# Optimization experiments

Hardware: AMD Instinct MI355X
Metric: run time of the kernel (lower is better)

## Reference

```python
import jax, jax.numpy as jnp
import numpy as np

N_NODES = 100000


def _gcn_layer(x, src, dst, W, b, num_nodes):
    # Linear transform first (PyG GCNConv applies Linear before propagate).
    h = x @ W.T  # [N, out]
    # Degree (with self loops already included in src/dst), computed on target.
    ones = jnp.ones(dst.shape[0], dtype=h.dtype)
    deg = jax.ops.segment_sum(ones, dst, num_segments=num_nodes)
    dinv = jnp.where(deg > 0, jax.lax.rsqrt(deg), 0.0)
    norm = dinv[src] * dinv[dst]  # [E]
    msg = h[src] * norm[:, None]  # gather + per-edge scale, [E, out]
    out = jax.ops.segment_sum(msg, dst, num_segments=num_nodes)
    return out + b


def setup_inputs() -> dict:
    key = jax.random.key(0)
    k1, k2, k3, k4, k5, k6 = jax.random.split(key, 6)
    d = 64
    x = jax.random.normal(k1, (N_NODES, d), dtype=jnp.float32)
    edge_index = jax.random.randint(k2, (2, 1600000), 0, N_NODES, dtype=jnp.int64)
    s = 1.0 / np.sqrt(d)
    W1 = jax.random.normal(k3, (d, d), dtype=jnp.float32) * s
    b1 = jax.random.normal(k4, (d,), dtype=jnp.float32) * 0.01
    W2 = jax.random.normal(k5, (d, d), dtype=jnp.float32) * s
    b2 = jax.random.normal(k6, (d,), dtype=jnp.float32) * 0.01
    return {"x": x, "edge_index": edge_index, "W1": W1, "b1": b1, "W2": W2, "b2": b2}


def reference(x, edge_index, W1, b1, W2, b2):
    n = x.shape[0]
    loop = jnp.arange(n, dtype=edge_index.dtype)
    src = jnp.concatenate([edge_index[0], loop])  # add self loops
    dst = jnp.concatenate([edge_index[1], loop])
    h = _gcn_layer(x, src, dst, W1, b1, n)
    out = _gcn_layer(h, src, dst, W2, b2, n)
    return out
```

## Files before the change

kernel.cpp:

```cpp
#include <hip/hip_runtime.h>
#include <hip/hip_fp16.h>


#define D 64
#define NPB 128
#define MAXB 784
#define CHUNK 4096
#define BT 512
#define CAP 3072

__global__ __launch_bounds__(BT) void build_scatter(const int* __restrict__ src,
                                                    const int* __restrict__ dst,
                                                    int* __restrict__ bcur,
                                                    int* __restrict__ entries0,
                                                    int nE, int B) {
    __shared__ int hist[MAXB];
    __shared__ int curs[MAXB];
    const int t = threadIdx.x;
    const int c = blockIdx.x;
    for (int b = t; b < B; b += BT) hist[b] = 0;
    __syncthreads();
    int e0 = c * CHUNK;
    int sv[CHUNK / BT], dv[CHUNK / BT];
#pragma unroll
    for (int i = 0; i < CHUNK / BT; ++i) {
        int e = e0 + i * BT + t;
        sv[i] = 0; dv[i] = -1;
        if (e < nE) {
            sv[i] = src[e];
            dv[i] = dst[e];
            atomicAdd(&hist[dv[i] >> 7], 1);
        }
    }
    __syncthreads();
    for (int b = t; b < B; b += BT) {
        int cnt = hist[b];
        int base = 0;
        if (cnt > 0) base = atomicAdd(&bcur[b], cnt);
        curs[b] = b * CAP + base;
    }
    __syncthreads();
#pragma unroll
    for (int i = 0; i < CHUNK / BT; ++i) {
        if (dv[i] >= 0) {
            int b = dv[i] >> 7;
            int pos = atomicAdd(&curs[b], 1);
            entries0[pos] = sv[i] | ((dv[i] & (NPB - 1)) << 17);
        }
    }
}

__device__ __forceinline__ void regroup_body(const int* __restrict__ entries0,
                                             int s0, int s1,
                                             int* __restrict__ off,
                                             int* __restrict__ deg,
                                             float* __restrict__ dinv,
                                             int* __restrict__ entries1,
                                             int* __restrict__ cursor, int N, int b,
                                             int* cnt, int* scn, int* cur, int* shb) {
    int t = threadIdx.x;
    if (t < NPB) cnt[t] = 0;
    if (t == 0) *shb = atomicAdd(cursor, s1 - s0);
    __syncthreads();
    for (int p = s0 + t; p < s1; p += 256)
        atomicAdd(&cnt[(entries0[p] >> 17) & (NPB - 1)], 1);
    __syncthreads();
    if (t < NPB) scn[t] = cnt[t];
    __syncthreads();
    for (int s = 1; s < NPB; s <<= 1) {
        int u = 0;
        if (t < NPB && t >= s) u = scn[t - s];
        __syncthreads();
        if (t < NPB) scn[t] += u;
        __syncthreads();
    }
    if (t < NPB) {
        int node = b * NPB + t;
        int c = cnt[t];
        int o = *shb + scn[t] - c;
        cur[t] = o;
        if (node < N) {
            off[node]  = o;
            deg[node]  = c;
            dinv[node] = rsqrtf((float)c + 1.0f);
        }
    }
    __syncthreads();
    for (int p = s0 + t; p < s1; p += 256) {
        int e = entries0[p];
        int pos = atomicAdd(&cur[(e >> 17) & (NPB - 1)], 1);
        entries1[pos] = e & 0x1FFFF;
    }
}

template <typename InT>
__device__ __forceinline__ void gemm_body(const InT* __restrict__ X,
                                          const float* __restrict__ W,
                                          const float* __restrict__ scale,
                                          __half* __restrict__ H, int N, int bx,
                                          float* xt, float* wt) {
    const int t = threadIdx.x;
    const int i0 = bx * 64;
#pragma unroll
    for (int r = 0; r < 16; ++r) {
        int idx = r * 256 + t;
        int j = idx >> 6, k = idx & 63;
        wt[k * 68 + j] = W[idx];
    }
#pragma unroll
    for (int r = 0; r < 16; ++r) {
        int idx = r * 256 + t;
        int i = idx >> 6, k = idx & 63;
        float v = 0.0f;
        if (i0 + i < N) {
            if constexpr (sizeof(InT) == 2)
                v = __half2float(((const __half*)X)[(size_t)(i0 + i) * D + k]);
            else
                v = ((const float*)X)[(size_t)(i0 + i) * D + k];
        }
        xt[k * 68 + i] = v;
    }
    __syncthreads();
    const int tn = (t & 15) * 4;
    const int tc = (t >> 4) * 4;
    float acc[4][4] = {};
#pragma unroll 8
    for (int k = 0; k < 64; ++k) {
        const float4 xa = *(const float4*)(xt + k * 68 + tn);
        const float4 wb = *(const float4*)(wt + k * 68 + tc);
        acc[0][0] += xa.x * wb.x; acc[0][1] += xa.x * wb.y; acc[0][2] += xa.x * wb.z; acc[0][3] += xa.x * wb.w;
        acc[1][0] += xa.y * wb.x; acc[1][1] += xa.y * wb.y; acc[1][2] += xa.y * wb.z; acc[1][3] += xa.y * wb.w;
        acc[2][0] += xa.z * wb.x; acc[2][1] += xa.z * wb.y; acc[2][2] += xa.z * wb.z; acc[2][3] += xa.z * wb.w;
        acc[3][0] += xa.w * wb.x; acc[3][1] += xa.w * wb.y; acc[3][2] += xa.w * wb.z; acc[3][3] += xa.w * wb.w;
    }
#pragma unroll
    for (int a = 0; a < 4; ++a) {
        int i = i0 + tn + a;
        if (i < N) {
            float sc = scale ? scale[i] : 1.0f;
            union { __half2 h2[2]; uint2 u2; } pk;
            pk.h2[0].x = __float2half_rn(acc[a][0] * sc);
            pk.h2[0].y = __float2half_rn(acc[a][1] * sc);
            pk.h2[1].x = __float2half_rn(acc[a][2] * sc);
            pk.h2[1].y = __float2half_rn(acc[a][3] * sc);
            *(uint2*)(&H[(size_t)i * D + tc]) = pk.u2;
        }
    }
}

__global__ __launch_bounds__(256) void regroup_gemm1(const int* __restrict__ entries0,
                                                     const int* __restrict__ btot,
                                                     int* __restrict__ off,
                                                     int* __restrict__ deg,
                                                     float* __restrict__ dinv,
                                                     int* __restrict__ entries1,
                                                     int* __restrict__ cursor,
                                                     int N, int B,
                                                     const float* __restrict__ X,
                                                     const float* __restrict__ W1,
                                                     __half* __restrict__ Hh) {
    __shared__ float xt[64 * 68];
    __shared__ float wt[64 * 68];
    if ((int)blockIdx.x < B) {
        int b = blockIdx.x;
        int* cnt = (int*)xt;
        int* scn = cnt + NPB;
        int* cur = scn + NPB;
        int* shb = cur + NPB;
        regroup_body(entries0, b * CAP, b * CAP + btot[b], off, deg, dinv,
                     entries1, cursor, N, b, cnt, scn, cur, shb);
    } else {
        gemm_body<float>(X, W1, nullptr, Hh, N, (int)blockIdx.x - B, xt, wt);
    }
}

template <bool PRESCALED>
__device__ __forceinline__ float2 agg_node(const int* __restrict__ csr, int beg, int end,
                                           const __half2* __restrict__ H2,
                                           const float* __restrict__ dinv,
                                           float dd, int p2, int h) {
    float2 acc = make_float2(0.0f, 0.0f);
    int p = beg;
    for (; p + 16 <= end; p += 16) {
        int s[8];
#pragma unroll
        for (int i = 0; i < 8; ++i) s[i] = csr[p + 2 * i + h];
        __half2 g[8];
#pragma unroll
        for (int i = 0; i < 8; ++i) g[i] = H2[(size_t)s[i] * 32 + p2];
        if constexpr (PRESCALED) {
#pragma unroll
            for (int i = 0; i < 8; ++i) {
                float2 f = __half22float2(g[i]);
                acc.x += f.x; acc.y += f.y;
            }
        } else {
            float dv[8];
#pragma unroll
            for (int i = 0; i < 8; ++i) dv[i] = dinv[s[i]];
#pragma unroll
            for (int i = 0; i < 8; ++i) {
                float2 f = __half22float2(g[i]);
                float c = dv[i] * dd;
                acc.x += f.x * c; acc.y += f.y * c;
            }
        }
    }
    for (; p + 8 <= end; p += 8) {
        int s0v = csr[p + 0 + h], s1v = csr[p + 2 + h];
        int s2v = csr[p + 4 + h], s3v = csr[p + 6 + h];
        __half2 g0 = H2[(size_t)s0v * 32 + p2];
        __half2 g1 = H2[(size_t)s1v * 32 + p2];
        __half2 g2 = H2[(size_t)s2v * 32 + p2];
        __half2 g3 = H2[(size_t)s3v * 32 + p2];
        float2 f0 = __half22float2(g0), f1 = __half22float2(g1);
        float2 f2 = __half22float2(g2), f3 = __half22float2(g3);
        if constexpr (PRESCALED) {
            acc.x += f0.x + f1.x + f2.x + f3.x;
            acc.y += f0.y + f1.y + f2.y + f3.y;
        } else {
            float c0 = dinv[s0v] * dd, c1 = dinv[s1v] * dd;
            float c2 = dinv[s2v] * dd, c3 = dinv[s3v] * dd;
            acc.x += f0.x * c0; acc.y += f0.y * c0;
            acc.x += f1.x * c1; acc.y += f1.y * c1;
            acc.x += f2.x * c2; acc.y += f2.y * c2;
            acc.x += f3.x * c3; acc.y += f3.y * c3;
        }
    }
    for (; p + 2 <= end; p += 2) {
        int s0v = csr[p + h];
        __half2 g0 = H2[(size_t)s0v * 32 + p2];
        float2 f0 = __half22float2(g0);
        if constexpr (PRESCALED) {
            acc.x += f0.x; acc.y += f0.y;
        } else {
            float c0 = dinv[s0v] * dd;
            acc.x += f0.x * c0; acc.y += f0.y * c0;
        }
    }
    if (p < end && h == 0) {
        int s0v = csr[p];
        __half2 g0 = H2[(size_t)s0v * 32 + p2];
        float2 f0 = __half22float2(g0);
        if constexpr (PRESCALED) {
            acc.x += f0.x; acc.y += f0.y;
        } else {
            float c0 = dinv[s0v] * dd;
            acc.x += f0.x * c0; acc.y += f0.y * c0;
        }
    }
    return acc;
}

template <typename OutT, bool PRESCALED>
__global__ __launch_bounds__(256) void aggregate3(const int* __restrict__ csr,
                                                  const int* __restrict__ off,
                                                  const int* __restrict__ deg,
                                                  const float* __restrict__ dinv,
                                                  const __half* __restrict__ H,
                                                  const float* __restrict__ bias,
                                                  OutT* __restrict__ out, int N) {
    int node = blockIdx.x * 4 + (threadIdx.x >> 6);
    if (node >= N) return;
    int lane = threadIdx.x & 63;
    int p2 = lane & 31;
    int h  = lane >> 5;
    const __half2* H2 = (const __half2*)H;
    float dd = dinv[node];
    int beg = off[node];
    int end = beg + deg[node];
    float2 acc = agg_node<PRESCALED>(csr, beg, end, H2, dinv, dd, p2, h);
    acc.x += __shfl_xor(acc.x, 32);
    acc.y += __shfl_xor(acc.y, 32);
    if (h == 0) {
        float2 hs = __half22float2(H2[(size_t)node * 32 + p2]);
        float2 bv = ((const float2*)bias)[p2];
        float2 o;
        if constexpr (PRESCALED) {
            o.x = (acc.x + hs.x) * dd + bv.x;
            o.y = (acc.y + hs.y) * dd + bv.y;
        } else {
            float s = dd * dd;
            o.x = acc.x + bv.x + hs.x * s;
            o.y = acc.y + bv.y + hs.y * s;
        }
        if constexpr (sizeof(OutT) == 2) {
            ((__half2*)(out + (size_t)node * D))[p2] = __float22half2_rn(o);
        } else {
            ((float2*)(out + (size_t)node * D))[p2] = o;
        }
    }
}

__global__ __launch_bounds__(256) void agg1_gemm2(const int* __restrict__ csr,
                                                  const int* __restrict__ off,
                                                  const int* __restrict__ deg,
                                                  const float* __restrict__ dinv,
                                                  const __half* __restrict__ H1,
                                                  const float* __restrict__ b1,
                                                  const float* __restrict__ W2,
                                                  __half* __restrict__ H2out, int N) {
    __shared__ float xt[64 * 68];
    __shared__ float wt[64 * 68];
    const int t = threadIdx.x;
#pragma unroll
    for (int r = 0; r < 16; ++r) {
        int idx = r * 256 + t;
        int j = idx >> 6, k = idx & 63;
        wt[k * 68 + j] = W2[idx];
    }
    const int i0 = blockIdx.x * 64;
    const int w = t >> 6, lane = t & 63, p2 = lane & 31, h = lane >> 5;
    const __half2* H2 = (const __half2*)H1;
    float2 bv = ((const float2*)b1)[p2];
    for (int r = 0; r < 16; ++r) {
        int il = w * 16 + r;
        int node = i0 + il;
        if (node < N) {
            float dd = dinv[node];
            int beg = off[node];
            int end = beg + deg[node];
            float2 acc = agg_node<false>(csr, beg, end, H2, dinv, dd, p2, h);
            acc.x += __shfl_xor(acc.x, 32);
            acc.y += __shfl_xor(acc.y, 32);
            if (h == 0) {
                float s = dd * dd;
                float2 hs = __half22float2(H2[(size_t)node * 32 + p2]);
                xt[(2 * p2)     * 68 + il] = acc.x + bv.x + hs.x * s;
                xt[(2 * p2 + 1) * 68 + il] = acc.y + bv.y + hs.y * s;
            }
        }
    }
    __syncthreads();
    const int tn = (t & 15) * 4;
    const int tc = (t >> 4) * 4;
    float acc[4][4] = {};
#pragma unroll 8
    for (int k = 0; k < 64; ++k) {
        const float4 xa = *(const float4*)(xt + k * 68 + tn);
        const float4 wb = *(const float4*)(wt + k * 68 + tc);
        acc[0][0] += xa.x * wb.x; acc[0][1] += xa.x * wb.y; acc[0][2] += xa.x * wb.z; acc[0][3] += xa.x * wb.w;
        acc[1][0] += xa.y * wb.x; acc[1][1] += xa.y * wb.y; acc[1][2] += xa.y * wb.z; acc[1][3] += xa.y * wb.w;
        acc[2][0] += xa.z * wb.x; acc[2][1] += xa.z * wb.y; acc[2][2] += xa.z * wb.z; acc[2][3] += xa.z * wb.w;
        acc[3][0] += xa.w * wb.x; acc[3][1] += xa.w * wb.y; acc[3][2] += xa.w * wb.z; acc[3][3] += xa.w * wb.w;
    }
#pragma unroll
    for (int a = 0; a < 4; ++a) {
        int i = i0 + tn + a;
        if (i < N) {
            float sc = dinv[i];
            union { __half2 h2[2]; uint2 u2; } pk;
            pk.h2[0].x = __float2half_rn(acc[a][0] * sc);
            pk.h2[0].y = __float2half_rn(acc[a][1] * sc);
            pk.h2[1].x = __float2half_rn(acc[a][2] * sc);
            pk.h2[1].y = __float2half_rn(acc[a][3] * sc);
            *(uint2*)(&H2out[(size_t)i * D + tc]) = pk.u2;
        }
    }
}

__global__ __launch_bounds__(256) void deg_kernel(const int* __restrict__ dst,
                                                  int* __restrict__ deg, int nE) {
    int e = blockIdx.x * 256 + threadIdx.x;
    if (e < nE) atomicAdd(&deg[dst[e]], 1);
}

__global__ __launch_bounds__(256) void dinv_kernel(const int* __restrict__ deg,
                                                   float* __restrict__ dinv, int N) {
    int i = blockIdx.x * 256 + threadIdx.x;
    if (i < N) dinv[i] = rsqrtf((float)deg[i] + 1.0f);
}

__global__ __launch_bounds__(256) void gemm_xwt(const float* __restrict__ X,
                                                const float* __restrict__ W,
                                                float* __restrict__ H, int N) {
    __shared__ float xt[64 * 68];
    __shared__ float wt[64 * 68];
    const int t = threadIdx.x;
    const int i0 = blockIdx.x * 64;
#pragma unroll
    for (int r = 0; r < 16; ++r) {
        int idx = r * 256 + t;
        int j = idx >> 6, k = idx & 63;
        wt[k * 68 + j] = W[idx];
    }
#pragma unroll
    for (int r = 0; r < 16; ++r) {
        int idx = r * 256 + t;
        int i = idx >> 6, k = idx & 63;
        float v = 0.0f;
        if (i0 + i < N) v = X[(size_t)(i0 + i) * D + k];
        xt[k * 68 + i] = v;
    }
    __syncthreads();
    const int tn = (t & 15) * 4;
    const int tc = (t >> 4) * 4;
    float acc[4][4] = {};
#pragma unroll 8
    for (int k = 0; k < 64; ++k) {
        const float4 xa = *(const float4*)(xt + k * 68 + tn);
        const float4 wb = *(const float4*)(wt + k * 68 + tc);
        acc[0][0] += xa.x * wb.x; acc[0][1] += xa.x * wb.y; acc[0][2] += xa.x * wb.z; acc[0][3] += xa.x * wb.w;
        acc[1][0] += xa.y * wb.x; acc[1][1] += xa.y * wb.y; acc[1][2] += xa.y * wb.z; acc[1][3] += xa.y * wb.w;
        acc[2][0] += xa.z * wb.x; acc[2][1] += xa.z * wb.y; acc[2][2] += xa.z * wb.z; acc[2][3] += xa.z * wb.w;
        acc[3][0] += xa.w * wb.x; acc[3][1] += xa.w * wb.y; acc[3][2] += xa.w * wb.z; acc[3][3] += xa.w * wb.w;
    }
#pragma unroll
    for (int a = 0; a < 4; ++a) {
        int i = i0 + tn + a;
        if (i < N) {
            float4 o = make_float4(acc[a][0], acc[a][1], acc[a][2], acc[a][3]);
            *(float4*)(H + (size_t)i * D + tc) = o;
        }
    }
}

__global__ __launch_bounds__(256) void init_out(const float* __restrict__ H,
                                                const float* __restrict__ dinv,
                                                const float* __restrict__ b,
                                                float* __restrict__ out, int N) {
    int idx4 = blockIdx.x * 256 + threadIdx.x;
    if (idx4 >= N * 16) return;
    int i = idx4 >> 4;
    int jc = idx4 & 15;
    float di = dinv[i];
    float s = di * di;
    float4 h4 = ((const float4*)H)[idx4];
    float4 b4 = ((const float4*)b)[jc];
    ((float4*)out)[idx4] = make_float4(b4.x + h4.x * s, b4.y + h4.y * s,
                                       b4.z + h4.z * s, b4.w + h4.w * s);
}

__global__ __launch_bounds__(256) void edge_scatter(const int* __restrict__ src,
                                                    const int* __restrict__ dst,
                                                    const float* __restrict__ dinv,
                                                    const float* __restrict__ H,
                                                    float* __restrict__ out, int nE) {
    int tid = blockIdx.x * 256 + threadIdx.x;
    int e = tid >> 4;
    if (e >= nE) return;
    int l = tid & 15;
    int s = src[e];
    int d = dst[e];
    float c = dinv[s] * dinv[d];
    float4 v = ((const float4*)H)[s * 16 + l];
    float* o = out + (size_t)d * D + l * 4;
    unsafeAtomicAdd(o + 0, v.x * c);
    unsafeAtomicAdd(o + 1, v.y * c);
    unsafeAtomicAdd(o + 2, v.z * c);
    unsafeAtomicAdd(o + 3, v.w * c);
}

static inline size_t align_up(size_t v, size_t a) { return (v + a - 1) & ~(a - 1); }

extern "C" void kernel_launch(void* const* d_in, const int* in_sizes, int n_in,
                              void* d_out, int out_size, void* d_ws, size_t ws_size,
                              hipStream_t stream) {
    const float* x  = (const float*)d_in[0];
    const int*   ei = (const int*)d_in[1];
    const float* W1 = (const float*)d_in[2];
    const float* b1 = (const float*)d_in[3];
    const float* W2 = (const float*)d_in[4];
    const float* b2 = (const float*)d_in[5];
    float* out = (float*)d_out;

    const int N  = in_sizes[0] / D;
    const int nE = in_sizes[1] / 2;
    const int* srcp = ei;
    const int* dstv = ei + nE;

    const int B = (N + NPB - 1) / NPB;
    const int C = (nE + CHUNK - 1) / CHUNK;

    char* base_p = (char*)d_ws;

    int gb_n = (N + 255) / 256;
    int gb_g = (N + 63) / 64;
    int gb_e = (nE + 255) / 256;
    int gb_a = (N + 3) / 4;

    size_t o = 0;
    int* bcur   = (int*)(base_p + o);
    int* cursor = bcur + B;
    o = align_up(o + (size_t)(B + 1) * 4, 256);
    int* off    = (int*)(base_p + o);   o = align_up(o + (size_t)N * 4, 256);
    int* deg    = (int*)(base_p + o);   o = align_up(o + (size_t)N * 4, 256);
    float* dinv = (float*)(base_p + o); o = align_up(o + (size_t)N * 4, 256);
    int* entries1 = (int*)(base_p + o); o = align_up(o + (size_t)nE * 4, 256);
    size_t rE0 = (size_t)MAXB * CAP * 4;
    size_t rH2 = (size_t)N * D * 2;
    size_t rX  = rE0 > rH2 ? rE0 : rH2;
    int* entries0 = (int*)(base_p + o);
    __half* H2h   = (__half*)(base_p + o);
    o = align_up(o + rX, 256);
    __half* Hh    = (__half*)(base_p + o);
    size_t need1 = o + align_up((size_t)N * D * 2, 256);

    if (ws_size >= need1 && B <= MAXB - 2) {
        hipMemsetAsync(bcur, 0, (size_t)(B + 1) * 4, stream);
        build_scatter<<<C, BT, 0, stream>>>(srcp, dstv, bcur, entries0, nE, B);
        regroup_gemm1<<<B + gb_g, 256, 0, stream>>>(entries0, bcur, off, deg,
                                                    dinv, entries1, cursor,
                                                    N, B, x, W1, Hh);
        agg1_gemm2<<<gb_g, 256, 0, stream>>>(entries1, off, deg, dinv, Hh, b1,
                                             W2, H2h, N);
        aggregate3<float, true><<<gb_a, 256, 0, stream>>>(entries1, off, deg, dinv,
                                                          H2h, b2, out, N);
    } else {
        size_t fo = 0;
        int* fdeg    = (int*)(base_p + fo);  fo = align_up(fo + (size_t)N * 4, 256);
        float* fdinv = (float*)(base_p + fo); fo = align_up(fo + (size_t)N * 4, 256);
        float* bufA  = (float*)(base_p + fo);
        hipMemsetAsync(fdeg, 0, (size_t)N * 4, stream);
        deg_kernel<<<gb_e, 256, 0, stream>>>(dstv, fdeg, nE);
        dinv_kernel<<<gb_n, 256, 0, stream>>>(fdeg, fdinv, N);
        int gb_i = (N * 16 + 255) / 256;
        int gb_e16 = (int)(((long long)nE * 16 + 255) / 256);
        gemm_xwt<<<gb_g, 256, 0, stream>>>(x, W1, bufA, N);
        init_out<<<gb_i, 256, 0, stream>>>(bufA, fdinv, b1, out, N);
        edge_scatter<<<gb_e16, 256, 0, stream>>>(srcp, dstv, fdinv, bufA, out, nE);
        gemm_xwt<<<gb_g, 256, 0, stream>>>(out, W2, bufA, N);
        init_out<<<gb_i, 256, 0, stream>>>(bufA, fdinv, b2, out, N);
        edge_scatter<<<gb_e16, 256, 0, stream>>>(srcp, dstv, fdinv, bufA, out, nE);
    }
}
```

Baseline: 297.2 us.

## Split fused layer-1 aggregation and GEMM2 into separate aggregate and GEMM kernels

Replaces the fused agg1_gemm2 kernel with a standalone aggregate3<__half,false> pass that writes the layer-1 output to a half buffer, followed by a separate templated gemm_xwt_h kernel that applies W2 and the dinv prescale. The fused kernel ran aggregation with only 4 waves per 64-node block, each wave handling 16 nodes serially, which likely limited parallelism for the memory-bound gather. The unfused path uses the 4-nodes-per-block aggregate grid for more parallelism, at the cost of an extra N x 64 half write and read plus one more kernel launch. The layer-2 H buffer now reuses the Hh buffer.

Result: faster. 274.5 us (median of 2 runs) (-7.6%).

```diff
diff --git a/kernel.cpp b/kernel.cpp
--- a/kernel.cpp
+++ b/kernel.cpp
@@ -146,6 +146,16 @@
             *(uint2*)(&H[(size_t)i * D + tc]) = pk.u2;
         }
     }
+}
+
+template <typename InT>
+__global__ __launch_bounds__(256) void gemm_xwt_h(const InT* __restrict__ X,
+                                                  const float* __restrict__ W,
+                                                  const float* __restrict__ scale,
+                                                  __half* __restrict__ H, int N) {
+    __shared__ float xt[64 * 68];
+    __shared__ float wt[64 * 68];
+    gemm_body<InT>(X, W, scale, H, N, blockIdx.x, xt, wt);
 }
 
 __global__ __launch_bounds__(256) void regroup_gemm1(const int* __restrict__ entries0,
@@ -292,73 +302,6 @@
     }
 }
 
-__global__ __launch_bounds__(256) void agg1_gemm2(const int* __restrict__ csr,
-                                                  const int* __restrict__ off,
-                                                  const int* __restrict__ deg,
-                                                  const float* __restrict__ dinv,
-                                                  const __half* __restrict__ H1,
-                                                  const float* __restrict__ b1,
-                                                  const float* __restrict__ W2,
-                                                  __half* __restrict__ H2out, int N) {
-    __shared__ float xt[64 * 68];
-    __shared__ float wt[64 * 68];
-    const int t = threadIdx.x;
-#pragma unroll
-    for (int r = 0; r < 16; ++r) {
-        int idx = r * 256 + t;
-        int j = idx >> 6, k = idx & 63;
-        wt[k * 68 + j] = W2[idx];
-    }
-    const int i0 = blockIdx.x * 64;
-    const int w = t >> 6, lane = t & 63, p2 = lane & 31, h = lane >> 5;
-    const __half2* H2 = (const __half2*)H1;
-    float2 bv = ((const float2*)b1)[p2];
-    for (int r = 0; r < 16; ++r) {
-        int il = w * 16 + r;
-        int node = i0 + il;
-        if (node < N) {
-            float dd = dinv[node];
-            int beg = off[node];
-            int end = beg + deg[node];
-            float2 acc = agg_node<false>(csr, beg, end, H2, dinv, dd, p2, h);
-            acc.x += __shfl_xor(acc.x, 32);
-            acc.y += __shfl_xor(acc.y, 32);
-            if (h == 0) {
-                float s = dd * dd;
-                float2 hs = __half22float2(H2[(size_t)node * 32 + p2]);
-                xt[(2 * p2)     * 68 + il] = acc.x + bv.x + hs.x * s;
-                xt[(2 * p2 + 1) * 68 + il] = acc.y + bv.y + hs.y * s;
-            }
-        }
-    }
-    __syncthreads();
-    const int tn = (t & 15) * 4;
-    const int tc = (t >> 4) * 4;
-    float acc[4][4] = {};
-#pragma unroll 8
-    for (int k = 0; k < 64; ++k) {
-        const float4 xa = *(const float4*)(xt + k * 68 + tn);
-        const float4 wb = *(const float4*)(wt + k * 68 + tc);
-        acc[0][0] += xa.x * wb.x; acc[0][1] += xa.x * wb.y; acc[0][2] += xa.x * wb.z; acc[0][3] += xa.x * wb.w;
-        acc[1][0] += xa.y * wb.x; acc[1][1] += xa.y * wb.y; acc[1][2] += xa.y * wb.z; acc[1][3] += xa.y * wb.w;
-        acc[2][0] += xa.z * wb.x; acc[2][1] += xa.z * wb.y; acc[2][2] += xa.z * wb.z; acc[2][3] += xa.z * wb.w;
-        acc[3][0] += xa.w * wb.x; acc[3][1] += xa.w * wb.y; acc[3][2] += xa.w * wb.z; acc[3][3] += xa.w * wb.w;
-    }
-#pragma unroll
-    for (int a = 0; a < 4; ++a) {
-        int i = i0 + tn + a;
-        if (i < N) {
-            float sc = dinv[i];
-            union { __half2 h2[2]; uint2 u2; } pk;
-            pk.h2[0].x = __float2half_rn(acc[a][0] * sc);
-            pk.h2[0].y = __float2half_rn(acc[a][1] * sc);
-            pk.h2[1].x = __float2half_rn(acc[a][2] * sc);
-            pk.h2[1].y = __float2half_rn(acc[a][3] * sc);
-            *(uint2*)(&H2out[(size_t)i * D + tc]) = pk.u2;
-        }
-    }
-}
-
 __global__ __launch_bounds__(256) void deg_kernel(const int* __restrict__ dst,
                                                   int* __restrict__ deg, int nE) {
     int e = blockIdx.x * 256 + threadIdx.x;
@@ -488,10 +431,10 @@
     float* dinv = (float*)(base_p + o); o = align_up(o + (size_t)N * 4, 256);
     int* entries1 = (int*)(base_p + o); o = align_up(o + (size_t)nE * 4, 256);
     size_t rE0 = (size_t)MAXB * CAP * 4;
-    size_t rH2 = (size_t)N * D * 2;
-    size_t rX  = rE0 > rH2 ? rE0 : rH2;
+    size_t rA1 = (size_t)N * D * 2;
+    size_t rX  = rE0 > rA1 ? rE0 : rA1;
     int* entries0 = (int*)(base_p + o);
-    __half* H2h   = (__half*)(base_p + o);
+    __half* A1h   = (__half*)(base_p + o);
     o = align_up(o + rX, 256);
     __half* Hh    = (__half*)(base_p + o);
     size_t need1 = o + align_up((size_t)N * D * 2, 256);
@@ -502,10 +445,11 @@
         regroup_gemm1<<<B + gb_g, 256, 0, stream>>>(entries0, bcur, off, deg,
                                                     dinv, entries1, cursor,
                                                     N, B, x, W1, Hh);
-        agg1_gemm2<<<gb_g, 256, 0, stream>>>(entries1, off, deg, dinv, Hh, b1,
-                                             W2, H2h, N);
+        aggregate3<__half, false><<<gb_a, 256, 0, stream>>>(entries1, off, deg, dinv,
+                                                            Hh, b1, A1h, N);
+        gemm_xwt_h<__half><<<gb_g, 256, 0, stream>>>(A1h, W2, dinv, Hh, N);
         aggregate3<float, true><<<gb_a, 256, 0, stream>>>(entries1, off, deg, dinv,
-                                                          H2h, b2, out, N);
+                                                          Hh, b2, out, N);
     } else {
         size_t fo = 0;
         int* fdeg    = (int*)(base_p + fo);  fo = align_up(fo + (size_t)N * 4, 256);
```
